# Kernel optimization log

Hardware: AMD Instinct MI355X
Metric: run time of the kernel (lower is better)

## Reference

```python
import jax, jax.numpy as jnp
import numpy as np

B, S, D, N, H, K = 32, 512, 2048, 16, 128, 64
EPS = 1e-6


def setup_inputs() -> dict:
    key = jax.random.key(0)
    ks = jax.random.split(key, 8)
    # glorot-uniform-like scale for the (D, N, H) attention kernels
    kern_scale = (6.0 / (D + H)) ** 0.5
    down_sd = 1.0 / K  # matches module: mean 0, sd = 1/downsampling_k
    q = jax.random.normal(ks[0], (B, S, D), dtype=jnp.float32)
    k = jax.random.normal(ks[1], (B, S, D), dtype=jnp.float32)
    v = jax.random.normal(ks[2], (B, S, D), dtype=jnp.float32)
    query_kernel = jax.random.uniform(ks[3], (D, N, H), jnp.float32, -kern_scale, kern_scale)
    key_kernel = jax.random.uniform(ks[4], (D, N, H), jnp.float32, -kern_scale, kern_scale)
    value_kernel = jax.random.uniform(ks[5], (D, N, H), jnp.float32, -kern_scale, kern_scale)
    key_down = down_sd * jax.random.normal(ks[6], (K, S), dtype=jnp.float32)
    value_down = down_sd * jax.random.normal(ks[7], (K, S), dtype=jnp.float32)
    return dict(q=q, k=k, v=v, query_kernel=query_kernel, key_kernel=key_kernel,
                value_kernel=value_kernel, key_down=key_down, value_down=value_down)


def reference(q, k, v, query_kernel, key_kernel, value_kernel, key_down, value_down):
    # Linformer-style downsampling of keys/values along the sequence axis: [B,S,D] -> [B,K,D]
    key_ds = jnp.einsum('ks,bsd->bkd', key_down, k)
    val_ds = jnp.einsum('ks,bsd->bkd', value_down, v)
    # Per-head projections
    queries = jnp.einsum('bqd,dnh->bqnh', q, query_kernel)   # [B,S,N,H]
    keys = jnp.einsum('bkd,dnh->bknh', key_ds, key_kernel)   # [B,K,N,H]
    values = jnp.einsum('bkd,dnh->bknh', val_ds, value_kernel)  # [B,K,N,H]
    # Kernelized linear attention with elu+1 feature map (mask=False branch)
    phi_q = jax.nn.elu(queries) + 1.0
    phi_k = jax.nn.elu(keys) + 1.0
    s = jnp.einsum('bknd,bknh->bndh', phi_k, values)  # [B,N,H,H]
    z = jnp.sum(phi_k, axis=1)                        # [B,N,H]
    qs = jnp.einsum('bqnd,bndh->bqnh', phi_q, s)      # [B,S,N,H]
    qz = jnp.einsum('bqnd,bnd->bqn', phi_q, z) + EPS  # [B,S,N]
    a_v = qs / qz[..., None]
    return a_v.reshape(B, S, N * H)
```

## Files before the change

### kernel.cpp

```cpp
#include <hip/hip_runtime.h>
#include <cstdint>
#include <cstddef>

typedef float f32x4 __attribute__((ext_vector_type(4)));
typedef short s16x8 __attribute__((ext_vector_type(8)));
typedef unsigned short u16;

#define EPS 1e-6f

__device__ __forceinline__ u16 f2bf(float f) {
    unsigned u = __float_as_uint(f);
    u += 0x7FFFu + ((u >> 16) & 1u);
    return (u16)(u >> 16);
}
__device__ __forceinline__ float bf2f(u16 u) {
    return __uint_as_float(((unsigned)u) << 16);
}

typedef const __attribute__((address_space(1))) void cg_void;
typedef __attribute__((address_space(3))) void l_void;
__device__ __forceinline__ void async16(void* dst_lds, const void* src_g) {
    __builtin_amdgcn_global_load_lds((cg_void*)src_g, (l_void*)dst_lds, 16, 0, 0);
}

#define BARRIER() do { asm volatile("" ::: "memory"); \
                       __builtin_amdgcn_s_barrier();  \
                       asm volatile("" ::: "memory"); } while (0)

__global__ __launch_bounds__(256) void prep_cast(
    const float* __restrict__ q, u16* __restrict__ qb,
    const float* __restrict__ w0, const float* __restrict__ w1,
    const float* __restrict__ w2, u16* __restrict__ o0,
    u16* __restrict__ o1, u16* __restrict__ o2)
{
    __shared__ u16 tl[64 * 68];
    const int bid = blockIdx.x;
    const int tid = threadIdx.x;
    if (bid < 3072) {
        int which = bid >> 10;
        int t = bid & 1023;
        const float* in = which == 0 ? w0 : which == 1 ? w1 : w2;
        u16* out        = which == 0 ? o0 : which == 1 ? o1 : o2;
        int bx = (t & 31) * 64, by = (t >> 5) * 64;
        int tx = tid & 63, ty = tid >> 6;
        #pragma unroll 4
        for (int i = ty; i < 64; i += 4)
            tl[tx * 68 + i] = f2bf(in[(size_t)(by + i) * 2048 + bx + tx]);
        __syncthreads();
        int srow = tid >> 2, sq = tid & 3;
        const u16* lp = &tl[srow * 68 + sq * 16];
        u16* op = &out[(size_t)(bx + srow) * 2048 + by + sq * 16];
        #pragma unroll
        for (int j8 = 0; j8 < 4; ++j8)
            *(short4*)(op + j8 * 4) = *(const short4*)(lp + j8 * 4);
    } else {
        int cb = bid - 3072;
        size_t base = (size_t)cb * 256 + tid;
        #pragma unroll
        for (int it = 0; it < 8; ++it) {
            size_t i = base + (size_t)it * 1048576;
            float4 f = ((const float4*)q)[i];
            ushort4 o;
            o.x = f2bf(f.x); o.y = f2bf(f.y); o.z = f2bf(f.z); o.w = f2bf(f.w);
            ((ushort4*)qb)[i] = o;
        }
    }
}

__global__ __launch_bounds__(256) void down_mfma(
    const float* __restrict__ kin, const float* __restrict__ vin,
    const float* __restrict__ wdk, const float* __restrict__ wdv,
    u16* __restrict__ kds, u16* __restrict__ vds)
{
    __shared__ __align__(16) u16 At[64 * 32];
    __shared__ __align__(16) u16 Bt[64 * 40];
    const int bid = blockIdx.x;
    const int tid = threadIdx.x;
    const int sel = bid >> 10, rem = bid & 1023;
    const int b = rem >> 5, d0 = (rem & 31) << 6;
    const float* x  = sel ? vin : kin;
    const float* wd = sel ? wdv : wdk;
    u16* outp       = sel ? vds : kds;
    const int w = tid >> 6, l = tid & 63, l16 = l & 15, k8 = l >> 4;
    f32x4 acc[4];
    #pragma unroll
    for (int fm = 0; fm < 4; ++fm) acc[fm] = (f32x4){0.f, 0.f, 0.f, 0.f};
    for (int s0 = 0; s0 < 512; s0 += 32) {
        __syncthreads();
        for (int c = tid; c < 512; c += 256) {
            int kkr = c >> 3, sc = (c & 7) << 2;
            float4 f = *(const float4*)&wd[kkr * 512 + s0 + sc];
            u16* dst = &At[kkr * 32 + sc];
            dst[0] = f2bf(f.x); dst[1] = f2bf(f.y); dst[2] = f2bf(f.z); dst[3] = f2bf(f.w);
        }
        {
            int c = tid;
            int sp = c >> 4, dq = (c & 15) << 2;
            int srow = sp << 1;
            const float* xp = &x[((size_t)(b * 512) + s0 + srow) * 2048 + d0 + dq];
            float4 f0 = *(const float4*)xp;
            float4 f1 = *(const float4*)(xp + 2048);
            int col = srow ^ ((c & 3) << 3);
            unsigned p0 = (unsigned)f2bf(f0.x) | ((unsigned)f2bf(f1.x) << 16);
            unsigned p1 = (unsigned)f2bf(f0.y) | ((unsigned)f2bf(f1.y) << 16);
            unsigned p2 = (unsigned)f2bf(f0.z) | ((unsigned)f2bf(f1.z) << 16);
            unsigned p3 = (unsigned)f2bf(f0.w) | ((unsigned)f2bf(f1.w) << 16);
            *(unsigned*)&Bt[(dq + 0) * 40 + col] = p0;
            *(unsigned*)&Bt[(dq + 1) * 40 + col] = p1;
            *(unsigned*)&Bt[(dq + 2) * 40 + col] = p2;
            *(unsigned*)&Bt[(dq + 3) * 40 + col] = p3;
        }
        __syncthreads();
        s16x8 af[4], bfr;
        #pragma unroll
        for (int fm = 0; fm < 4; ++fm)
            af[fm] = *(const s16x8*)&At[(fm * 16 + l16) * 32 + k8 * 8];
        bfr = *(const s16x8*)&Bt[((w << 4) + l16) * 40 + ((k8 ^ (l16 >> 2)) << 3)];
        #pragma unroll
        for (int fm = 0; fm < 4; ++fm)
            acc[fm] = __builtin_amdgcn_mfma_f32_16x16x32_bf16(af[fm], bfr, acc[fm], 0, 0, 0);
    }
    #pragma unroll
    for (int fm = 0; fm < 4; ++fm)
        #pragma unroll
        for (int j = 0; j < 4; ++j) {
            int r = fm * 16 + k8 * 4 + j;
            int c = (w << 4) + l16;
            outp[((size_t)(b * 64 + r)) * 2048 + d0 + c] = f2bf(acc[fm][j]);
        }
}

__global__ __launch_bounds__(256) void gemm128_dual(
    const u16* __restrict__ A0, const u16* __restrict__ B0, u16* __restrict__ C0,
    const u16* __restrict__ A1, const u16* __restrict__ B1, u16* __restrict__ C1)
{
    const u16* A  = blockIdx.z ? A1 : A0;
    const u16* BT = blockIdx.z ? B1 : B0;
    u16* C        = blockIdx.z ? C1 : C0;
    const bool elu = (blockIdx.z == 0);
    const int K = 2048;

    __shared__ __align__(16) u16 lds[2][8192];
    const int tid = threadIdx.x;
    const int w = tid >> 6, l = tid & 63;
    const int wm = w >> 1, wn = w & 1;
    const int l16 = l & 15, k8 = l >> 4;
    const int sr = (w << 4) + (l >> 2);
    const int sc = (l & 3) << 3;
    const int row0 = blockIdx.y * 128, col0 = blockIdx.x * 128;
    const int nk = K >> 5;
    f32x4 acc[4][4] = {};

#define STAGE(buf, kt) do {                                                        \
        int kk0 = (kt) << 5;                                                       \
        _Pragma("unroll")                                                          \
        for (int i = 0; i < 2; ++i) {                                              \
            const u16* ga = A + (size_t)(row0 + i * 64 + sr) * K + kk0 + sc;       \
            async16(&lds[buf][i * 2048 + (w << 9)], ga);                           \
            const u16* gb = BT + (size_t)(col0 + i * 64 + sr) * K + kk0 + sc;      \
            async16(&lds[buf][4096 + i * 2048 + (w << 9)], gb);                    \
        }                                                                          \
    } while (0)

    STAGE(0, 0);
    asm volatile("s_waitcnt vmcnt(0)" ::: "memory");
    __syncthreads();
    int cur = 0;
    for (int kt = 0; kt < nk; ++kt) {
        if (kt + 1 < nk) STAGE(cur ^ 1, kt + 1);
        s16x8 af[4], bfr[4];
        const u16* Ab = &lds[cur][0];
        const u16* Bb = &lds[cur][4096];
        #pragma unroll
        for (int fm = 0; fm < 4; ++fm)
            af[fm] = *(const s16x8*)&Ab[((wm << 6) + (fm << 4) + l16) * 32 + (k8 << 3)];
        #pragma unroll
        for (int fn = 0; fn < 4; ++fn)
            bfr[fn] = *(const s16x8*)&Bb[((wn << 6) + (fn << 4) + l16) * 32 + (k8 << 3)];
        #pragma unroll
        for (int fm = 0; fm < 4; ++fm)
            #pragma unroll
            for (int fn = 0; fn < 4; ++fn)
                acc[fm][fn] = __builtin_amdgcn_mfma_f32_16x16x32_bf16(af[fm], bfr[fn], acc[fm][fn], 0, 0, 0);
        __syncthreads();
        cur ^= 1;
    }
#undef STAGE

    #pragma unroll
    for (int fm = 0; fm < 4; ++fm)
        #pragma unroll
        for (int j = 0; j < 4; ++j) {
            int r = row0 + (wm << 6) + (fm << 4) + (k8 << 2) + j;
            size_t rbase = (size_t)r * 2048;
            #pragma unroll
            for (int fn = 0; fn < 4; ++fn) {
                int c = col0 + (wn << 6) + (fn << 4) + l16;
                float x = acc[fm][fn][j];
                if (elu) x = x > 0.0f ? x + 1.0f : __expf(x);
                C[rbase + c] = f2bf(x);
            }
        }
}

__global__ __launch_bounds__(256) void sz_kernel(
    const u16* __restrict__ phik, const u16* __restrict__ vals,
    u16* __restrict__ sT, float* __restrict__ z)
{
    int b = blockIdx.x >> 4, n = blockIdx.x & 15;
    __shared__ __align__(16) u16 pk[64 * 128];
    __shared__ __align__(16) u16 vv[64 * 128];
    int tid = threadIdx.x;
    for (int i = tid; i < 1024; i += 256) {
        int r = i >> 4, c8 = (i & 15) << 3;
        size_t g = ((size_t)(b * 64 + r)) * 2048 + n * 128 + c8;
        ((s16x8*)pk)[i] = *(const s16x8*)&phik[g];
        ((s16x8*)vv)[i] = *(const s16x8*)&vals[g];
    }
    __syncthreads();
    if (tid < 128) {
        float s = 0.0f;
        for (int kk = 0; kk < 64; ++kk) s += bf2f(pk[kk * 128 + tid]);
        z[((size_t)(b * 16 + n)) * 128 + tid] = s;
    }
    int hg = tid >> 4, dg = tid & 15;
    int h0 = hg * 8, d0 = dg * 8;
    float acc[8][8] = {};
    for (int kk = 0; kk < 64; ++kk) {
        s16x8 vr = *(const s16x8*)&vv[kk * 128 + h0];
        s16x8 pr = *(const s16x8*)&pk[kk * 128 + d0];
        float va[8], pa[8];
        #pragma unroll
        for (int i = 0; i < 8; ++i) { va[i] = bf2f((u16)vr[i]); pa[i] = bf2f((u16)pr[i]); }
        #pragma unroll
        for (int i = 0; i < 8; ++i)
            #pragma unroll
            for (int j = 0; j < 8; ++j)
                acc[i][j] += va[i] * pa[j];
    }
    size_t base = ((size_t)(b * 16 + n)) * 16384;
    #pragma unroll
    for (int i = 0; i < 8; ++i) {
        u16 row[8];
        #pragma unroll
        for (int j = 0; j < 8; ++j) row[j] = f2bf(acc[i][j]);
        *(s16x8*)&sT[base + (size_t)(h0 + i) * 128 + d0] = *(s16x8*)row;
    }
}

__global__ __launch_bounds__(512, 2) void gemm256_qs(
    const u16* __restrict__ A, const u16* __restrict__ BT,
    const u16* __restrict__ sT, const float* __restrict__ z,
    float* __restrict__ outp)
{
    const int K = 2048, N = 2048, NT = 32, nbn = 8;
    __shared__ __align__(16) u16 lds[8][8192];
    const int tid = threadIdx.x;
    const int w = tid >> 6, l = tid & 63;
    const int wm = w >> 2, wn = w & 3;
    const int l16 = l & 15, k8 = l >> 4;

    const int nwg = gridDim.x;
    int wg = blockIdx.x;
    if ((nwg & 7) == 0) wg = (wg & 7) * (nwg >> 3) + (wg >> 3);
    const int row0 = (wg / nbn) << 8, col0 = (wg % nbn) << 8;

    const int lr  = l >> 3;
    const int scb = (((l & 7) ^ lr) << 4);
    const int swzr = (l16 & 7) << 4;

#define PANEL(s, m, h) (&lds[((s) << 2) | ((m) << 1) | (h)][0])

#define STG(pan, G, prow0, kk0) do {                                             \
        _Pragma("unroll")                                                        \
        for (int i_ = 0; i_ < 2; ++i_) {                                         \
            int seg_ = w + (i_ << 3);                                            \
            const u16* src_ = (G) + (size_t)((prow0) + (seg_ << 3) + lr) * K     \
                              + (kk0) + (scb >> 1);                              \
            async16((pan) + (seg_ << 9), src_);                                  \
        } } while (0)

#define LDA(slot, mh) do { const u16* p_ = PANEL(slot, 0, mh);                   \
        _Pragma("unroll")                                                        \
        for (int fm_ = 0; fm_ < 4; ++fm_)                                        \
        _Pragma("unroll")                                                        \
        for (int ks_ = 0; ks_ < 2; ++ks_)                                        \
            Af[fm_][ks_] = *(const s16x8*)(p_ + (wm * 64 + fm_ * 16 + l16) * 64  \
                           + (((ks_ * 64 + k8 * 16) ^ swzr) >> 1)); } while (0)

#define LDB(slot, nh, dst) do { const u16* p_ = PANEL(slot, 1, nh);              \
        _Pragma("unroll")                                                        \
        for (int fn_ = 0; fn_ < 2; ++fn_)                                        \
        _Pragma("unroll")                                                        \
        for (int ks_ = 0; ks_ < 2; ++ks_)                                        \
            dst[fn_][ks_] = *(const s16x8*)(p_ + (wn * 32 + fn_ * 16 + l16) * 64 \
                           + (((ks_ * 64 + k8 * 16) ^ swzr) >> 1)); } while (0)

#define MM(mh, nh, BF) do {                                                      \
        __builtin_amdgcn_s_setprio(1);                                           \
        _Pragma("unroll")                                                        \
        for (int fm_ = 0; fm_ < 4; ++fm_)                                        \
        _Pragma("unroll")                                                        \
        for (int fn_ = 0; fn_ < 2; ++fn_)                                        \
        _Pragma("unroll")                                                        \
        for (int ks_ = 0; ks_ < 2; ++ks_)                                        \
            acc[mh][nh][fm_][fn_] = __builtin_amdgcn_mfma_f32_16x16x32_bf16(     \
                Af[fm_][ks_], BF[fn_][ks_], acc[mh][nh][fm_][fn_], 0, 0, 0);     \
        __builtin_amdgcn_s_setprio(0); } while (0)

#define TILE(t, cur, nxt, BFc, BFn) do {                                         \
        LDA(cur, 0);                                                             \
        if ((t) + 1 < NT) STG(PANEL(nxt, 0, 1), A, row0 + 128, ((t) + 1) << 6);  \
        BARRIER(); MM(0, 0, BFc); BARRIER();                                     \
        LDB(cur, 1, Bf1);                                                        \
        if ((t) + 2 < NT) STG(PANEL(cur, 0, 0), A, row0, ((t) + 2) << 6);        \
        BARRIER(); MM(0, 1, Bf1); BARRIER();                                     \
        LDA(cur, 1);                                                             \
        if ((t) + 2 < NT) STG(PANEL(cur, 1, 0), BT, col0, ((t) + 2) << 6);       \
        BARRIER(); MM(1, 1, Bf1); BARRIER();                                     \
        if ((t) + 2 < NT) STG(PANEL(cur, 1, 1), BT, col0 + 128, ((t) + 2) << 6); \
        BARRIER(); MM(1, 0, BFc);                                                \
        if ((t) == NT - 2)     asm volatile("s_waitcnt vmcnt(0)" ::: "memory");  \
        else if ((t) < NT - 2) asm volatile("s_waitcnt vmcnt(6)" ::: "memory");  \
        BARRIER();                                                               \
        if ((t) + 1 < NT) LDB(nxt, 0, BFn);                                      \
    } while (0)

    f32x4 acc[2][2][4][2] = {};
    s16x8 Af[4][2], Bf0a[2][2], Bf0b[2][2], Bf1[2][2];

    STG(PANEL(0, 0, 0), A,  row0,       0);
    STG(PANEL(0, 1, 0), BT, col0,       0);
    STG(PANEL(0, 1, 1), BT, col0 + 128, 0);
    STG(PANEL(0, 0, 1), A,  row0 + 128, 0);
    STG(PANEL(1, 0, 0), A,  row0,       64);
    STG(PANEL(1, 1, 0), BT, col0,       64);
    STG(PANEL(1, 1, 1), BT, col0 + 128, 64);
    asm volatile("s_waitcnt vmcnt(6)" ::: "memory");
    BARRIER();
    LDB(0, 0, Bf0a);

    for (int t = 0; t < NT; t += 2) {
        TILE(t,     0, 1, Bf0a, Bf0b);
        TILE(t + 1, 1, 0, Bf0b, Bf0a);
    }
#undef PANEL
#undef STG
#undef LDA
#undef LDB
#undef MM
#undef TILE

    const int b = row0 >> 9;
    const int n0 = col0 >> 7;
    u16* P = &lds[0][0];

    #pragma unroll
    for (int mh = 0; mh < 2; ++mh)
        #pragma unroll
        for (int fm = 0; fm < 4; ++fm)
            #pragma unroll
            for (int j = 0; j < 4; ++j) {
                int rr = mh * 128 + wm * 64 + fm * 16 + k8 * 4 + j;
                int rowbase = rr * 256;
                int msk = ((rr >> 2) & 7) << 4;
                #pragma unroll
                for (int nh = 0; nh < 2; ++nh)
                    #pragma unroll
                    for (int fn = 0; fn < 2; ++fn) {
                        int cc = nh * 128 + wn * 32 + fn * 16 + l16;
                        float x = acc[mh][nh][fm][fn][j];
                        x = x > 0.0f ? x + 1.0f : __expf(x);
                        P[rowbase + (cc ^ msk)] = f2bf(x);
                    }
            }
    __syncthreads();

    for (int nsel = 0; nsel < 2; ++nsel) {
        const int nn = n0 + nsel;
        const size_t stb = ((size_t)(b * 16 + nn)) << 14;
        const float* zp0 = z + ((size_t)(b * 16 + nn) << 7);

        s16x8 Bz[4];
        #pragma unroll
        for (int ks = 0; ks < 4; ++ks) {
            const float* zp = zp0 + (ks << 5) + (k8 << 3);
            float4 f0 = *(const float4*)zp;
            float4 f1 = *(const float4*)(zp + 4);
            u16 tmp[8] = { f2bf(f0.x), f2bf(f0.y), f2bf(f0.z), f2bf(f0.w),
                           f2bf(f1.x), f2bf(f1.y), f2bf(f1.z), f2bf(f1.w) };
            Bz[ks] = *(const s16x8*)tmp;
        }

        s16x8 Af2[2][4];
        #pragma unroll
        for (int fm2 = 0; fm2 < 2; ++fm2) {
            int rr = (w << 5) + (fm2 << 4) + l16;
            int rowbase = rr * 256;
            int msk = ((rr >> 2) & 7) << 4;
            #pragma unroll
            for (int ks = 0; ks < 4; ++ks) {
                int cc = (nsel << 7) + (ks << 5) + (k8 << 3);
                Af2[fm2][ks] = *(const s16x8*)&P[rowbase + (cc ^ msk)];
            }
        }

        f32x4 accz[2] = {};
        #pragma unroll
        for (int fm2 = 0; fm2 < 2; ++fm2)
            #pragma unroll
            for (int ks = 0; ks < 4; ++ks)
                accz[fm2] = __builtin_amdgcn_mfma_f32_16x16x32_bf16(Af2[fm2][ks], Bz[ks], accz[fm2], 0, 0, 0);

        f32x4 acc2[2][8] = {};
        #pragma unroll
        for (int fn = 0; fn < 8; ++fn) {
            s16x8 Bfr[4];
            #pragma unroll
            for (int ks = 0; ks < 4; ++ks)
                Bfr[ks] = *(const s16x8*)&sT[stb + (size_t)((fn << 4) + l16) * 128
                                             + (ks << 5) + (k8 << 3)];
            #pragma unroll
            for (int fm2 = 0; fm2 < 2; ++fm2)
                #pragma unroll
                for (int ks = 0; ks < 4; ++ks)
                    acc2[fm2][fn] = __builtin_amdgcn_mfma_f32_16x16x32_bf16(Af2[fm2][ks], Bfr[ks], acc2[fm2][fn], 0, 0, 0);
        }

        #pragma unroll
        for (int fm2 = 0; fm2 < 2; ++fm2)
            #pragma unroll
            for (int j = 0; j < 4; ++j) {
                int grow = row0 + (w << 5) + (fm2 << 4) + (k8 << 2) + j;
                float rq = 1.0f / (accz[fm2][j] + EPS);
                size_t ob = (size_t)grow * 2048 + col0 + (nsel << 7);
                #pragma unroll
                for (int fn = 0; fn < 8; ++fn)
                    outp[ob + (fn << 4) + l16] = acc2[fm2][fn][j] * rq;
            }
    }
}

extern "C" void kernel_launch(void* const* d_in, const int* in_sizes, int n_in,
                              void* d_out, int out_size, void* d_ws, size_t ws_size,
                              hipStream_t stream) {
    (void)in_sizes; (void)n_in; (void)out_size; (void)ws_size;
    const float* q   = (const float*)d_in[0];
    const float* k   = (const float*)d_in[1];
    const float* v   = (const float*)d_in[2];
    const float* wq  = (const float*)d_in[3];
    const float* wk  = (const float*)d_in[4];
    const float* wv  = (const float*)d_in[5];
    const float* kdw = (const float*)d_in[6];
    const float* vdw = (const float*)d_in[7];
    float* out = (float*)d_out;

    char* p = (char*)d_ws;
    u16* qb   = (u16*)p; p += (size_t)16384 * 2048 * 2;
    u16* wqT  = (u16*)p; p += (size_t)2048 * 2048 * 2;
    u16* wkT  = (u16*)p; p += (size_t)2048 * 2048 * 2;
    u16* wvT  = (u16*)p; p += (size_t)2048 * 2048 * 2;
    u16* kds  = (u16*)p; p += (size_t)2048 * 2048 * 2;
    u16* vds  = (u16*)p; p += (size_t)2048 * 2048 * 2;
    u16* phik = (u16*)p; p += (size_t)2048 * 2048 * 2;
    u16* vals = (u16*)p; p += (size_t)2048 * 2048 * 2;
    u16* sT   = (u16*)p; p += (size_t)512 * 128 * 128 * 2;
    float* z  = (float*)p; p += (size_t)512 * 128 * 4;

    prep_cast<<<7168, 256, 0, stream>>>(q, qb, wq, wk, wv, wqT, wkT, wvT);
    down_mfma<<<2048, 256, 0, stream>>>(k, v, kdw, vdw, kds, vds);
    gemm128_dual<<<dim3(16, 16, 2), 256, 0, stream>>>(kds, wkT, phik, vds, wvT, vals);
    sz_kernel<<<512, 256, 0, stream>>>(phik, vals, sT, z);
    gemm256_qs<<<512, 512, 0, stream>>>(qb, wqT, sT, z, out);
}
```

Measured before the change: 374.7 us.

## Merge prep and downsample kernels; stage per-head sT tile in LDS for qs epilogue

Merges the cast/transpose prep kernel and the sequence-downsampling MFMA kernel into one launch, with the downsample blocks scheduled first, so the two can overlap and one launch disappears. In the final GEMM epilogue, the phi(q) tile is written to LDS one head-half at a time, and the 128x128 sT block for that head is loaded into LDS with async global-to-LDS copies using an XOR swizzle. The MFMA B fragments are then read from LDS instead of directly from global memory. This adds barriers per head-half and mixes different block types in one grid, which can affect occupancy.

```diff
diff --git a/kernel.cpp b/kernel.cpp
--- a/kernel.cpp
+++ b/kernel.cpp
@@ -27,18 +27,79 @@
                        __builtin_amdgcn_s_barrier();  \
                        asm volatile("" ::: "memory"); } while (0)
 
-__global__ __launch_bounds__(256) void prep_cast(
+__global__ __launch_bounds__(256) void prep_down(
     const float* __restrict__ q, u16* __restrict__ qb,
     const float* __restrict__ w0, const float* __restrict__ w1,
     const float* __restrict__ w2, u16* __restrict__ o0,
-    u16* __restrict__ o1, u16* __restrict__ o2)
+    u16* __restrict__ o1, u16* __restrict__ o2,
+    const float* __restrict__ kin, const float* __restrict__ vin,
+    const float* __restrict__ wdk, const float* __restrict__ wdv,
+    u16* __restrict__ kds, u16* __restrict__ vds)
 {
-    __shared__ u16 tl[64 * 68];
+    __shared__ __align__(16) char smem[9216];
     const int bid = blockIdx.x;
     const int tid = threadIdx.x;
-    if (bid < 3072) {
-        int which = bid >> 10;
-        int t = bid & 1023;
+
+    if (bid < 2048) {
+        u16* At = (u16*)smem;
+        u16* Bt = (u16*)(smem + 4096);
+        const int sel = bid >> 10, rem = bid & 1023;
+        const int b = rem >> 5, d0 = (rem & 31) << 6;
+        const float* x  = sel ? vin : kin;
+        const float* wd = sel ? wdv : wdk;
+        u16* outp       = sel ? vds : kds;
+        const int w = tid >> 6, l = tid & 63, l16 = l & 15, k8 = l >> 4;
+        f32x4 acc[4];
+        #pragma unroll
+        for (int fm = 0; fm < 4; ++fm) acc[fm] = (f32x4){0.f, 0.f, 0.f, 0.f};
+        for (int s0 = 0; s0 < 512; s0 += 32) {
+            __syncthreads();
+            for (int c = tid; c < 512; c += 256) {
+                int kkr = c >> 3, sc = (c & 7) << 2;
+                float4 f = *(const float4*)&wd[kkr * 512 + s0 + sc];
+                u16* dst = &At[kkr * 32 + sc];
+                dst[0] = f2bf(f.x); dst[1] = f2bf(f.y); dst[2] = f2bf(f.z); dst[3] = f2bf(f.w);
+            }
+            {
+                int c = tid;
+                int sp = c >> 4, dq = (c & 15) << 2;
+                int srow = sp << 1;
+                const float* xp = &x[((size_t)(b * 512) + s0 + srow) * 2048 + d0 + dq];
+                float4 f0 = *(const float4*)xp;
+                float4 f1 = *(const float4*)(xp + 2048);
+                int col = srow ^ ((c & 3) << 3);
+                unsigned p0 = (unsigned)f2bf(f0.x) | ((unsigned)f2bf(f1.x) << 16);
+                unsigned p1 = (unsigned)f2bf(f0.y) | ((unsigned)f2bf(f1.y) << 16);
+                unsigned p2 = (unsigned)f2bf(f0.z) | ((unsigned)f2bf(f1.z) << 16);
+                unsigned p3 = (unsigned)f2bf(f0.w) | ((unsigned)f2bf(f1.w) << 16);
+                *(unsigned*)&Bt[(dq + 0) * 40 + col] = p0;
+                *(unsigned*)&Bt[(dq + 1) * 40 + col] = p1;
+                *(unsigned*)&Bt[(dq + 2) * 40 + col] = p2;
+                *(unsigned*)&Bt[(dq + 3) * 40 + col] = p3;
+            }
+            __syncthreads();
+            s16x8 af[4], bfr;
+            #pragma unroll
+            for (int fm = 0; fm < 4; ++fm)
+                af[fm] = *(const s16x8*)&At[(fm * 16 + l16) * 32 + k8 * 8];
+            bfr = *(const s16x8*)&Bt[((w << 4) + l16) * 40 + ((k8 ^ (l16 >> 2)) << 3)];
+            #pragma unroll
+            for (int fm = 0; fm < 4; ++fm)
+                acc[fm] = __builtin_amdgcn_mfma_f32_16x16x32_bf16(af[fm], bfr, acc[fm], 0, 0, 0);
+        }
+        #pragma unroll
+        for (int fm = 0; fm < 4; ++fm)
+            #pragma unroll
+            for (int j = 0; j < 4; ++j) {
+                int r = fm * 16 + k8 * 4 + j;
+                int c = (w << 4) + l16;
+                outp[((size_t)(b * 64 + r)) * 2048 + d0 + c] = f2bf(acc[fm][j]);
+            }
+    } else if (bid < 5120) {
+        u16* tl = (u16*)smem;
+        int wb = bid - 2048;
+        int which = wb >> 10;
+        int t = wb & 1023;
         const float* in = which == 0 ? w0 : which == 1 ? w1 : w2;
         u16* out        = which == 0 ? o0 : which == 1 ? o1 : o2;
         int bx = (t & 31) * 64, by = (t >> 5) * 64;
@@ -54,7 +115,7 @@
         for (int j8 = 0; j8 < 4; ++j8)
             *(short4*)(op + j8 * 4) = *(const short4*)(lp + j8 * 4);
     } else {
-        int cb = bid - 3072;
+        int cb = bid - 5120;
         size_t base = (size_t)cb * 256 + tid;
         #pragma unroll
         for (int it = 0; it < 8; ++it) {
@@ -65,69 +126,6 @@
             ((ushort4*)qb)[i] = o;
         }
     }
-}
-
-__global__ __launch_bounds__(256) void down_mfma(
-    const float* __restrict__ kin, const float* __restrict__ vin,
-    const float* __restrict__ wdk, const float* __restrict__ wdv,
-    u16* __restrict__ kds, u16* __restrict__ vds)
-{
-    __shared__ __align__(16) u16 At[64 * 32];
-    __shared__ __align__(16) u16 Bt[64 * 40];
-    const int bid = blockIdx.x;
-    const int tid = threadIdx.x;
-    const int sel = bid >> 10, rem = bid & 1023;
-    const int b = rem >> 5, d0 = (rem & 31) << 6;
-    const float* x  = sel ? vin : kin;
-    const float* wd = sel ? wdv : wdk;
-    u16* outp       = sel ? vds : kds;
-    const int w = tid >> 6, l = tid & 63, l16 = l & 15, k8 = l >> 4;
-    f32x4 acc[4];
-    #pragma unroll
-    for (int fm = 0; fm < 4; ++fm) acc[fm] = (f32x4){0.f, 0.f, 0.f, 0.f};
-    for (int s0 = 0; s0 < 512; s0 += 32) {
-        __syncthreads();
-        for (int c = tid; c < 512; c += 256) {
-            int kkr = c >> 3, sc = (c & 7) << 2;
-            float4 f = *(const float4*)&wd[kkr * 512 + s0 + sc];
-            u16* dst = &At[kkr * 32 + sc];
-            dst[0] = f2bf(f.x); dst[1] = f2bf(f.y); dst[2] = f2bf(f.z); dst[3] = f2bf(f.w);
-        }
-        {
-            int c = tid;
-            int sp = c >> 4, dq = (c & 15) << 2;
-            int srow = sp << 1;
-            const float* xp = &x[((size_t)(b * 512) + s0 + srow) * 2048 + d0 + dq];
-            float4 f0 = *(const float4*)xp;
-            float4 f1 = *(const float4*)(xp + 2048);
-            int col = srow ^ ((c & 3) << 3);
-            unsigned p0 = (unsigned)f2bf(f0.x) | ((unsigned)f2bf(f1.x) << 16);
-            unsigned p1 = (unsigned)f2bf(f0.y) | ((unsigned)f2bf(f1.y) << 16);
-            unsigned p2 = (unsigned)f2bf(f0.z) | ((unsigned)f2bf(f1.z) << 16);
-            unsigned p3 = (unsigned)f2bf(f0.w) | ((unsigned)f2bf(f1.w) << 16);
-            *(unsigned*)&Bt[(dq + 0) * 40 + col] = p0;
-            *(unsigned*)&Bt[(dq + 1) * 40 + col] = p1;
-            *(unsigned*)&Bt[(dq + 2) * 40 + col] = p2;
-            *(unsigned*)&Bt[(dq + 3) * 40 + col] = p3;
-        }
-        __syncthreads();
-        s16x8 af[4], bfr;
-        #pragma unroll
-        for (int fm = 0; fm < 4; ++fm)
-            af[fm] = *(const s16x8*)&At[(fm * 16 + l16) * 32 + k8 * 8];
-        bfr = *(const s16x8*)&Bt[((w << 4) + l16) * 40 + ((k8 ^ (l16 >> 2)) << 3)];
-        #pragma unroll
-        for (int fm = 0; fm < 4; ++fm)
-            acc[fm] = __builtin_amdgcn_mfma_f32_16x16x32_bf16(af[fm], bfr, acc[fm], 0, 0, 0);
-    }
-    #pragma unroll
-    for (int fm = 0; fm < 4; ++fm)
-        #pragma unroll
-        for (int j = 0; j < 4; ++j) {
-            int r = fm * 16 + k8 * 4 + j;
-            int c = (w << 4) + l16;
-            outp[((size_t)(b * 64 + r)) * 2048 + d0 + c] = f2bf(acc[fm][j]);
-        }
 }
 
 __global__ __launch_bounds__(256) void gemm128_dual(
@@ -253,7 +251,7 @@
     const u16* __restrict__ sT, const float* __restrict__ z,
     float* __restrict__ outp)
 {
-    const int K = 2048, N = 2048, NT = 32, nbn = 8;
+    const int K = 2048, NT = 32, nbn = 8;
     __shared__ __align__(16) u16 lds[8][8192];
     const int tid = threadIdx.x;
     const int w = tid >> 6, l = tid & 63;
@@ -353,34 +351,43 @@
 
     const int b = row0 >> 9;
     const int n0 = col0 >> 7;
-    u16* P = &lds[0][0];
+    u16* Ph  = &lds[0][0];
+    u16* sTl = &lds[4][0];
 
     #pragma unroll
-    for (int mh = 0; mh < 2; ++mh)
-        #pragma unroll
-        for (int fm = 0; fm < 4; ++fm)
-            #pragma unroll
-            for (int j = 0; j < 4; ++j) {
-                int rr = mh * 128 + wm * 64 + fm * 16 + k8 * 4 + j;
-                int rowbase = rr * 256;
-                int msk = ((rr >> 2) & 7) << 4;
+    for (int nsel = 0; nsel < 2; ++nsel) {
+        #pragma unroll
+        for (int mh = 0; mh < 2; ++mh)
+            #pragma unroll
+            for (int fm = 0; fm < 4; ++fm)
                 #pragma unroll
-                for (int nh = 0; nh < 2; ++nh)
+                for (int j = 0; j < 4; ++j) {
+                    int rr = mh * 128 + wm * 64 + fm * 16 + k8 * 4 + j;
+                    int rowbase = rr << 7;
+                    int msk = ((rr >> 2) & 7) << 4;
                     #pragma unroll
                     for (int fn = 0; fn < 2; ++fn) {
-                        int cc = nh * 128 + wn * 32 + fn * 16 + l16;
-                        float x = acc[mh][nh][fm][fn][j];
+                        int cc = wn * 32 + fn * 16 + l16;
+                        float x = acc[mh][nsel][fm][fn][j];
                         x = x > 0.0f ? x + 1.0f : __expf(x);
-                        P[rowbase + (cc ^ msk)] = f2bf(x);
+                        Ph[rowbase + (cc ^ msk)] = f2bf(x);
                     }
-            }
-    __syncthreads();
-
-    for (int nsel = 0; nsel < 2; ++nsel) {
+                }
+        {
+            const size_t stb = ((size_t)(b * 16 + n0 + nsel)) << 14;
+            #pragma unroll
+            for (int it = 0; it < 4; ++it) {
+                int g = (it << 12) + (tid << 3);
+                int row = g >> 7;
+                int ch8 = (g >> 3) & 15;
+                const u16* src = sT + stb + (row << 7) + ((ch8 ^ (row & 7)) << 3);
+                async16(&sTl[g], src);
+            }
+        }
+        __syncthreads();
+
         const int nn = n0 + nsel;
-        const size_t stb = ((size_t)(b * 16 + nn)) << 14;
         const float* zp0 = z + ((size_t)(b * 16 + nn) << 7);
-
         s16x8 Bz[4];
         #pragma unroll
         for (int ks = 0; ks < 4; ++ks) {
@@ -396,12 +403,12 @@
         #pragma unroll
         for (int fm2 = 0; fm2 < 2; ++fm2) {
             int rr = (w << 5) + (fm2 << 4) + l16;
-            int rowbase = rr * 256;
+            int rowbase = rr << 7;
             int msk = ((rr >> 2) & 7) << 4;
             #pragma unroll
             for (int ks = 0; ks < 4; ++ks) {
-                int cc = (nsel << 7) + (ks << 5) + (k8 << 3);
-                Af2[fm2][ks] = *(const s16x8*)&P[rowbase + (cc ^ msk)];
+                int cc = (ks << 5) + (k8 << 3);
+                Af2[fm2][ks] = *(const s16x8*)&Ph[rowbase + (cc ^ msk)];
             }
         }
 
@@ -417,9 +424,11 @@
         for (int fn = 0; fn < 8; ++fn) {
             s16x8 Bfr[4];
             #pragma unroll
-            for (int ks = 0; ks < 4; ++ks)
-                Bfr[ks] = *(const s16x8*)&sT[stb + (size_t)((fn << 4) + l16) * 128
-                                             + (ks << 5) + (k8 << 3)];
+            for (int ks = 0; ks < 4; ++ks) {
+                int rw = (fn << 4) + l16;
+                Bfr[ks] = *(const s16x8*)&sTl[(rw << 7)
+                            + (((ks << 5) + (k8 << 3)) ^ ((rw & 7) << 3))];
+            }
             #pragma unroll
             for (int fm2 = 0; fm2 < 2; ++fm2)
                 #pragma unroll
@@ -438,6 +447,7 @@
                 for (int fn = 0; fn < 8; ++fn)
                     outp[ob + (fn << 4) + l16] = acc2[fm2][fn][j] * rq;
             }
+        __syncthreads();
     }
 }
 
@@ -467,8 +477,8 @@
     u16* sT   = (u16*)p; p += (size_t)512 * 128 * 128 * 2;
     float* z  = (float*)p; p += (size_t)512 * 128 * 4;
 
-    prep_cast<<<7168, 256, 0, stream>>>(q, qb, wq, wk, wv, wqT, wkT, wvT);
-    down_mfma<<<2048, 256, 0, stream>>>(k, v, kdw, vdw, kds, vds);
+    prep_down<<<9216, 256, 0, stream>>>(q, qb, wq, wk, wv, wqT, wkT, wvT,
+                                        k, v, kdw, vdw, kds, vds);
     gemm128_dual<<<dim3(16, 16, 2), 256, 0, stream>>>(kds, wkT, phik, vds, wvT, vals);
     sz_kernel<<<512, 256, 0, stream>>>(phik, vals, sT, z);
     gemm256_qs<<<512, 512, 0, stream>>>(qb, wqT, sT, z, out);
```

New measurement: 344.7 us, median of 2. -8.0%, faster.
